# Performance work log

Measured on AMD Instinct MI355X. Metric: run time of the kernel, lower is better.

## Reference

```python
import jax, jax.numpy as jnp
import numpy as np

D_MODEL, HQ, HKV = 2048, 32, 8
DK = D_MODEL // HQ          # 64
GROUP = HQ // HKV           # 4 query heads per kv head
B, S = 1, 2048


def setup_inputs() -> dict:
    key = jax.random.key(0)
    ks = jax.random.split(key, 5)
    sc = 0.02
    return {
        "x":  jax.random.normal(ks[0], (B, S, D_MODEL), jnp.float32),
        "wq": jax.random.normal(ks[1], (D_MODEL, D_MODEL), jnp.float32) * sc,
        "bq": jnp.zeros((D_MODEL,), jnp.float32),
        "wk": jax.random.normal(ks[2], (HKV * DK, D_MODEL), jnp.float32) * sc,
        "bk": jnp.zeros((HKV * DK,), jnp.float32),
        "wv": jax.random.normal(ks[3], (HKV * DK, D_MODEL), jnp.float32) * sc,
        "bv": jnp.zeros((HKV * DK,), jnp.float32),
        "wo": jax.random.normal(ks[4], (D_MODEL, D_MODEL), jnp.float32) * sc,
        "bo": jnp.zeros((D_MODEL,), jnp.float32),
    }


def reference(x, wq, bq, wk, bk, wv, bv, wo, bo):
    b, s, _ = x.shape
    scale = 1.0 / jnp.sqrt(jnp.asarray(DK, x.dtype))
    # projections (torch Linear: y = x @ W.T + b)
    q = (x @ wq.T + bq).reshape(b, s, HKV, GROUP, DK)   # [B,S,Hkv,G,Dk]
    k = (x @ wk.T + bk).reshape(b, s, HKV, DK)          # [B,S,Hkv,Dk]
    v = (x @ wv.T + bv).reshape(b, s, HKV, DK)
    # GQA: broadcast each kv head over its GROUP query heads (no repeat_interleave)
    scores = jnp.einsum("bshgd,bthd->bhgst", q, k) * scale   # [B,Hkv,G,S,S]
    causal = jnp.tril(jnp.ones((s, s), bool))
    scores = jnp.where(causal, scores, jnp.asarray(-jnp.inf, scores.dtype))
    attn = jax.nn.softmax(scores, axis=-1)
    out = jnp.einsum("bhgst,bthd->bshgd", attn, v)           # [B,S,Hkv,G,Dk]
    out = out.reshape(b, s, D_MODEL)
    return out @ wo.T + bo
```

## Files before the change

kernel.cpp:

```cpp
#include <hip/hip_runtime.h>


#define S_LEN 2048
#define DM    2048
#define QKVW  3072

typedef float  f32x4  __attribute__((ext_vector_type(4)));
typedef float  f32x16 __attribute__((ext_vector_type(16)));
typedef __bf16 bf16x8 __attribute__((ext_vector_type(8)));
typedef unsigned short u16;
typedef unsigned int   u32;
typedef u16 u16x8 __attribute__((ext_vector_type(8)));
typedef u32 u32x4 __attribute__((ext_vector_type(4)));

__device__ __forceinline__ u16 f2b(float f) {
    __bf16 h = (__bf16)f;
    return __builtin_bit_cast(unsigned short, h);
}
__device__ __forceinline__ u32 pk2(float lo, float hi) {
    return (u32)f2b(lo) | ((u32)f2b(hi) << 16);
}
__device__ __forceinline__ float max3f(float a, float b, float c) {
    return fmaxf(fmaxf(a, b), c);
}

#define MFMA16(a, b, c) __builtin_amdgcn_mfma_f32_16x16x32_bf16((a), (b), (c), 0, 0, 0)
#define MFMA32(a, b, c) __builtin_amdgcn_mfma_f32_32x32x16_bf16((a), (b), (c), 0, 0, 0)

__device__ __forceinline__ void gld16(const void* g, void* l) {
    __builtin_amdgcn_global_load_lds(
        (const __attribute__((address_space(1))) void*)g,
        (__attribute__((address_space(3))) void*)l, 16, 0, 0);
}

__global__ __launch_bounds__(256) void cvt5(
    const float* __restrict__ x,  const float* __restrict__ wq,
    const float* __restrict__ wk, const float* __restrict__ wv,
    const float* __restrict__ wo,
    const float* __restrict__ bq, const float* __restrict__ bk,
    const float* __restrict__ bv,
    u16* __restrict__ xb, u16* __restrict__ wqkvb, u16* __restrict__ wob,
    float* __restrict__ bqkv)
{
    if (blockIdx.x == 7168) {
        for (int i = threadIdx.x; i < 3072; i += 256)
            bqkv[i] = (i < 2048) ? bq[i] : (i < 2560 ? bk[i - 2048] : bv[i - 2560]);
        return;
    }
    int i = blockIdx.x * 256 + threadIdx.x;
    const float* s; u16* d; int off;
    if      (i < 524288)  { s = x;  d = xb;    off = i; }
    else if (i < 1048576) { s = wq; d = wqkvb; off = i - 524288; }
    else if (i < 1179648) { s = wk; d = wqkvb + (size_t)2048 * 2048; off = i - 1048576; }
    else if (i < 1310720) { s = wv; d = wqkvb + (size_t)2560 * 2048; off = i - 1179648; }
    else                  { s = wo; d = wob;   off = i - 1310720; }
    const float4* s4 = (const float4*)s;
    float4 a = s4[2 * (size_t)off], b = s4[2 * (size_t)off + 1];
    u16x8 o;
    o[0] = f2b(a.x); o[1] = f2b(a.y); o[2] = f2b(a.z); o[3] = f2b(a.w);
    o[4] = f2b(b.x); o[5] = f2b(b.y); o[6] = f2b(b.z); o[7] = f2b(b.w);
    ((u16x8*)d)[(size_t)off] = o;
}

template <bool OUT_BF16, bool QSCALE>
__global__ __launch_bounds__(256) void gemm_nt64(
    const u16* __restrict__ A, const u16* __restrict__ B,
    const float* __restrict__ bias, void* __restrict__ Cv,
    int N, int K, int nxb)
{
    __shared__ u16 As[2][128 * 32];
    __shared__ u16 Bs[2][64 * 32];
    const int nwg = gridDim.x;
    const int bid = blockIdx.x;
    const int wg  = (bid & 7) * (nwg >> 3) + (bid >> 3);
    const int bm  = (wg / nxb) * 128;
    const int bn  = (wg % nxb) * 64;

    const int tid  = threadIdx.x;
    const int lane = tid & 63;
    const int w    = tid >> 6;
    const int wr   = w >> 1, wc = w & 1;
    const int la = lane & 15, lg = lane >> 4;

    f32x4 acc[4][2] = {};

    char* const abase = (char*)&As[0][0] + w * 1024;
    char* const bbase = (char*)&Bs[0][0] + w * 1024;

    for (int k0 = 0; k0 < K; k0 += 64) {
        #pragma unroll
        for (int i = 0; i < 4; ++i) {
            const int c   = tid + 256 * i;
            const int kh  = c >> 9;
            const int rem = c & 511;
            const int row = rem >> 2;
            const int seg = rem & 3;
            gld16(A + (size_t)(bm + row) * K + k0 + kh * 32 + seg * 8,
                  abase + i * 4096);
        }
        #pragma unroll
        for (int i = 0; i < 2; ++i) {
            const int c   = tid + 256 * i;
            const int kh  = c >> 8;
            const int rem = c & 255;
            const int row = rem >> 2;
            const int seg = rem & 3;
            gld16(B + (size_t)(bn + row) * K + k0 + kh * 32 + seg * 8,
                  bbase + i * 4096);
        }
        __syncthreads();
        #pragma unroll
        for (int kh = 0; kh < 2; ++kh) {
            bf16x8 af[4], bf[2];
            #pragma unroll
            for (int m = 0; m < 4; ++m)
                af[m] = *(const bf16x8*)(&As[kh][0] + (wr * 64 + m * 16 + la) * 32 + lg * 8);
            #pragma unroll
            for (int n = 0; n < 2; ++n)
                bf[n] = *(const bf16x8*)(&Bs[kh][0] + (wc * 32 + n * 16 + la) * 32 + lg * 8);
            #pragma unroll
            for (int m = 0; m < 4; ++m)
                #pragma unroll
                for (int n = 0; n < 2; ++n)
                    acc[m][n] = MFMA16(af[m], bf[n], acc[m][n]);
        }
        __syncthreads();
    }

    #pragma unroll
    for (int m = 0; m < 4; ++m) {
        #pragma unroll
        for (int n = 0; n < 2; ++n) {
            const int col = bn + wc * 32 + n * 16 + la;
            const float bb = bias[col];
            const float osc = (QSCALE && col < 2048) ? 0.180336881f : 1.0f;
            #pragma unroll
            for (int j = 0; j < 4; ++j) {
                const int row = bm + wr * 64 + m * 16 + lg * 4 + j;
                const float v = (acc[m][n][j] + bb) * osc;
                if (OUT_BF16) ((u16*)Cv)[(size_t)row * N + col] = f2b(v);
                else          ((float*)Cv)[(size_t)row * N + col] = v;
            }
        }
    }
}

__global__ __launch_bounds__(256) void kvrepack(const u16* __restrict__ QKVb,
                                                u16* __restrict__ Kp,
                                                u16* __restrict__ Vt) {
    const int h   = blockIdx.y;
    const int kt  = blockIdx.x;
    const int tid = threadIdx.x;
    __shared__ u16 T[64][72];
    #pragma unroll
    for (int p = 0; p < 2; ++p) {
        const int idx = p * 256 + tid;
        const int r   = idx >> 3;
        const int c8  = (idx & 7) * 8;
        *(u16x8*)&Kp[((size_t)h * S_LEN + kt * 64 + r) * 64 + c8] =
            *(const u16x8*)&QKVb[(size_t)(kt * 64 + r) * QKVW + 2048 + h * 64 + c8];
    }
    #pragma unroll
    for (int p = 0; p < 2; ++p) {
        const int r  = p * 32 + (tid >> 3);
        const int cs = (tid & 7) * 8;
        u16x8 v = *(const u16x8*)&QKVb[(size_t)(kt * 64 + r) * QKVW + 2560 + h * 64 + cs];
        #pragma unroll
        for (int j = 0; j < 8; ++j) T[r][cs + j] = v[j];
    }
    __syncthreads();
    #pragma unroll
    for (int p = 0; p < 2; ++p) {
        const int d  = p * 32 + (tid >> 3);
        const int ks = (tid & 7) * 8;
        u16x8 o;
        #pragma unroll
        for (int j = 0; j < 8; ++j) o[j] = T[ks + j][d];
        *(u16x8*)&Vt[((size_t)h * 64 + d) * S_LEN + kt * 64 + ks] = o;
    }
}

__global__ __launch_bounds__(512, 4) void attn(
    const u16* __restrict__ Qb,
    const u16* __restrict__ Kp,
    const u16* __restrict__ Vt,
    u16* __restrict__ Ob)
{
    const int tid  = threadIdx.x;
    const int lane = tid & 63;
    const int w    = tid >> 6;
    const int head = w & 3;
    const int par  = w >> 2;
    const int bid  = blockIdx.x;
    const int band = (bid < 256) ? (63 - (bid >> 3)) : ((bid - 256) >> 3);
    const int h    = bid & 7;
    const int hq   = h * 4 + head;
    const int q0   = band * 32;
    const int lq   = lane & 31;
    const int hi   = lane >> 5;

    __shared__ char LDS[65536];

    bf16x8 qf[4];
    #pragma unroll
    for (int ds = 0; ds < 4; ++ds)
        qf[ds] = *(const bf16x8*)&Qb[(size_t)(q0 + lq) * QKVW + hq * 64 + ds * 16 + hi * 8];

    f32x16 ot[2] = {};
    float m = -3e38f, lsum = 0.f;

    const char* Khb = (const char*)(Kp + (size_t)h * S_LEN * 64);
    const char* Vhb = (const char*)(Vt + (size_t)h * 64 * S_LEN);

    const int r0 = tid >> 3;
    const int s0 = (((tid & 7) ^ (r0 & 7)) << 4);
    const int woff = w * 1024;

    const int nch = (band >> 1) + 1;
    const int nit = (nch + 1) >> 1;

    auto stage_pair = [&](int j) {
        const int pb = (j & 1) * 16384;
        const size_t kr = (size_t)(j * 128 + r0);
        gld16(Khb + (kr << 7) + s0,          LDS + pb + woff);
        gld16(Khb + ((kr + 64) << 7) + s0,   LDS + pb + 8192 + woff);
        const size_t vb = ((size_t)r0 << 12) + (size_t)(j * 256) + s0;
        gld16(Vhb + vb,        LDS + 32768 + pb + woff);
        gld16(Vhb + vb + 128,  LDS + 32768 + pb + 8192 + woff);
    };

    stage_pair(0);
    __syncthreads();

    for (int i = 0; i < nit; ++i) {
        if (i + 1 < nit) stage_pair(i + 1);

        const int cg = 2 * i + par;
        if (cg < nch) {
            const int base = (i & 1) * 16384 + par * 8192;
            const char* Kb = LDS + base;
            const char* Vb = LDS + 32768 + base;
            const int k0 = cg * 64;

            f32x16 s[2];
            __builtin_amdgcn_s_setprio(1);
            #pragma unroll
            for (int kt = 0; kt < 2; ++kt) {
                f32x16 acc = {};
                #pragma unroll
                for (int ds = 0; ds < 4; ++ds) {
                    const int key = kt * 32 + lq;
                    const int byteK = (key << 7) + ((ds * 32 + hi * 16) ^ ((key & 7) << 4));
                    bf16x8 kf = *(const bf16x8*)(Kb + byteK);
                    acc = MFMA32(kf, qf[ds], acc);
                }
                s[kt] = acc;
            }
            __builtin_amdgcn_s_setprio(0);

            if (k0 + 63 > q0) {
                #pragma unroll
                for (int kt = 0; kt < 2; ++kt)
                    #pragma unroll
                    for (int r = 0; r < 16; ++r) {
                        const int key = k0 + kt * 32 + (r & 3) + 8 * (r >> 2) + 4 * hi;
                        if (key > q0 + lq) s[kt][r] = -1e30f;
                    }
            }

            float t10[11];
            #pragma unroll
            for (int r = 0; r < 10; ++r)
                t10[r] = max3f(s[(3*r) >> 4][(3*r) & 15],
                               s[(3*r+1) >> 4][(3*r+1) & 15],
                               s[(3*r+2) >> 4][(3*r+2) & 15]);
            t10[10] = fmaxf(s[1][14], s[1][15]);
            const float x0 = max3f(t10[0], t10[1], t10[2]);
            const float x1 = max3f(t10[3], t10[4], t10[5]);
            const float x2 = max3f(t10[6], t10[7], t10[8]);
            const float x3 = fmaxf(t10[9], t10[10]);
            float pm = fmaxf(max3f(x0, x1, x2), x3);
            pm = fmaxf(pm, __shfl_xor(pm, 32));

            if (!__all(pm <= m + 11.5f)) {
                const float mn   = fmaxf(m, pm);
                const float corr = __builtin_exp2f(m - mn);
                m = mn;
                lsum *= corr;
                #pragma unroll
                for (int r = 0; r < 16; ++r) {
                    const int row = (r & 3) + 8 * (r >> 2) + 4 * hi;
                    const float cr = __shfl(corr, row);
                    ot[0][r] *= cr;
                    ot[1][r] *= cr;
                }
            }

            float ps = 0.f;
            #pragma unroll
            for (int kt = 0; kt < 2; ++kt)
                #pragma unroll
                for (int r = 0; r < 16; ++r) {
                    const float p = __builtin_exp2f(s[kt][r] - m);
                    s[kt][r] = p;
                    ps += p;
                }
            lsum += ps + __shfl_xor(ps, 32);

            bf16x8 pa[4];
            #pragma unroll
            for (int kb = 0; kb < 4; ++kb) {
                const int kt = kb >> 1;
                const int rb = (kb & 1) * 8;
                const u32 A = pk2(s[kt][rb + 0], s[kt][rb + 1]);
                const u32 B = pk2(s[kt][rb + 4], s[kt][rb + 5]);
                const u32 C = pk2(s[kt][rb + 2], s[kt][rb + 3]);
                const u32 D = pk2(s[kt][rb + 6], s[kt][rb + 7]);
                const u32 sA = __shfl_xor(A, 32), sB = __shfl_xor(B, 32);
                const u32 sC = __shfl_xor(C, 32), sD = __shfl_xor(D, 32);
                u32x4 t4;
                t4[0] = hi ? sB : A;
                t4[1] = hi ? sD : C;
                t4[2] = hi ? B : sA;
                t4[3] = hi ? D : sC;
                pa[kb] = __builtin_bit_cast(bf16x8, t4);
            }

            __builtin_amdgcn_s_setprio(1);
            #pragma unroll
            for (int dt = 0; dt < 2; ++dt)
                #pragma unroll
                for (int kb = 0; kb < 4; ++kb) {
                    const int d = dt * 32 + lq;
                    const int byteV = (d << 7) + ((kb * 32 + hi * 16) ^ ((d & 7) << 4));
                    bf16x8 vf = *(const bf16x8*)(Vb + byteV);
                    ot[dt] = MFMA32(pa[kb], vf, ot[dt]);
                }
            __builtin_amdgcn_s_setprio(0);
        }

        __syncthreads();
    }

    float* Uls = (float*)LDS;
    float* Mls = (float*)(LDS + 32768);
    float* Lls = (float*)(LDS + 33280);

    if (par == 1) {
        #pragma unroll
        for (int r = 0; r < 16; ++r) {
            const int row = (r & 3) + 8 * (r >> 2) + 4 * hi;
            Uls[(head * 32 + row) * 64 + lq]      = ot[0][r];
            Uls[(head * 32 + row) * 64 + 32 + lq] = ot[1][r];
        }
        if (lane < 32) { Mls[head * 32 + lane] = m; Lls[head * 32 + lane] = lsum; }
    }
    __syncthreads();
    if (par == 1) return;

    const float m1  = Mls[head * 32 + lq];
    const float l1  = Lls[head * 32 + lq];
    const float M   = fmaxf(m, m1);
    const float a0  = __builtin_exp2f(m - M);
    const float a1  = __builtin_exp2f(m1 - M);
    const float inv = 1.f / (a0 * lsum + a1 * l1);

    #pragma unroll
    for (int r = 0; r < 16; ++r) {
        const int row = (r & 3) + 8 * (r >> 2) + 4 * hi;
        const float a0r = __shfl(a0, row);
        const float a1r = __shfl(a1, row);
        const float ivr = __shfl(inv, row);
        #pragma unroll
        for (int dt = 0; dt < 2; ++dt) {
            const float u1 = Uls[(head * 32 + row) * 64 + dt * 32 + lq];
            Ob[(size_t)(q0 + row) * DM + hq * 64 + dt * 32 + lq] =
                f2b((a0r * ot[dt][r] + a1r * u1) * ivr);
        }
    }
}

extern "C" void kernel_launch(void* const* d_in, const int* in_sizes, int n_in,
                              void* d_out, int out_size, void* d_ws, size_t ws_size,
                              hipStream_t stream)
{
    const float* x  = (const float*)d_in[0];
    const float* wq = (const float*)d_in[1];
    const float* bq = (const float*)d_in[2];
    const float* wk = (const float*)d_in[3];
    const float* bk = (const float*)d_in[4];
    const float* wv = (const float*)d_in[5];
    const float* bv = (const float*)d_in[6];
    const float* wo = (const float*)d_in[7];
    const float* bo = (const float*)d_in[8];
    float* out = (float*)d_out;

    char* ws = (char*)d_ws;
    u16* xb     = (u16*)(ws);
    u16* wqkvb  = (u16*)(ws + (8u  << 20));
    u16* wob    = (u16*)(ws + (20u << 20));
    u16* QKVb   = (u16*)(ws + (28u << 20));
    float* bqkv = (float*)(ws + (40u << 20));
    u16* Ob = xb;
    u16* Kp = wqkvb;
    u16* Vt = wqkvb + (size_t)2 * 1024 * 1024 / 2;

    cvt5<<<7169, 256, 0, stream>>>(x, wq, wk, wv, wo, bq, bk, bv,
                                   xb, wqkvb, wob, bqkv);
    gemm_nt64<true, true><<<768, 256, 0, stream>>>(
        xb, wqkvb, bqkv, QKVb, QKVW, 2048, QKVW / 64);
    kvrepack<<<dim3(32, 8), 256, 0, stream>>>(QKVb, Kp, Vt);
    attn<<<512, 512, 0, stream>>>(QKVb, Kp, Vt, Ob);
    gemm_nt64<false, false><<<512, 256, 0, stream>>>(
        Ob, wob, bo, out, DM, 2048, DM / 64);
}
```

Before: 137.6 us.

## Read K directly from QKV buffer and use permlane32 swap for half-wave exchanges

Removes the K repack from the repack kernel, so attention stages K tiles straight from the strided QKV projection output (row stride 6144 bytes) instead of a packed per-head copy. Separately, it replaces the cross-half-wave __shfl_xor(…,32) exchanges in the softmax max, sum and P-fragment build with the permlane32_swap builtin when available. This saves a copy pass and some LDS-routed shuffles, but the K loads become strided global reads with less locality.

```diff
diff --git a/kernel.cpp b/kernel.cpp
--- a/kernel.cpp
+++ b/kernel.cpp
@@ -12,6 +12,7 @@
 typedef unsigned int   u32;
 typedef u16 u16x8 __attribute__((ext_vector_type(8)));
 typedef u32 u32x4 __attribute__((ext_vector_type(4)));
+typedef u32 u32x2 __attribute__((ext_vector_type(2)));
 
 __device__ __forceinline__ u16 f2b(float f) {
     __bf16 h = (__bf16)f;
@@ -22,6 +23,28 @@
 }
 __device__ __forceinline__ float max3f(float a, float b, float c) {
     return fmaxf(fmaxf(a, b), c);
+}
+
+__device__ __forceinline__ void xswap(u32 a, u32 b, u32& lo, u32& hi) {
+#if __has_builtin(__builtin_amdgcn_permlane32_swap)
+    u32x2 r = __builtin_amdgcn_permlane32_swap(a, b, false, false);
+    lo = r[0]; hi = r[1];
+#else
+    const int hf = (threadIdx.x & 63) >> 5;
+    const u32 sA = __shfl_xor(a, 32), sB = __shfl_xor(b, 32);
+    lo = hf ? sB : a;
+    hi = hf ? b : sA;
+#endif
+}
+__device__ __forceinline__ float xhalf_max(float x) {
+    u32 xb = __builtin_bit_cast(u32, x), lo, hi;
+    xswap(xb, xb, lo, hi);
+    return fmaxf(__builtin_bit_cast(float, lo), __builtin_bit_cast(float, hi));
+}
+__device__ __forceinline__ float xhalf_sum(float x) {
+    u32 xb = __builtin_bit_cast(u32, x), lo, hi;
+    xswap(xb, xb, lo, hi);
+    return __builtin_bit_cast(float, lo) + __builtin_bit_cast(float, hi);
 }
 
 #define MFMA16(a, b, c) __builtin_amdgcn_mfma_f32_16x16x32_bf16((a), (b), (c), 0, 0, 0)
@@ -145,23 +168,14 @@
     }
 }
 
-__global__ __launch_bounds__(256) void kvrepack(const u16* __restrict__ QKVb,
-                                                u16* __restrict__ Kp,
-                                                u16* __restrict__ Vt) {
+__global__ __launch_bounds__(256) void vrepack(const u16* __restrict__ QKVb,
+                                               u16* __restrict__ Vt) {
     const int h   = blockIdx.y;
     const int kt  = blockIdx.x;
     const int tid = threadIdx.x;
     __shared__ u16 T[64][72];
     #pragma unroll
     for (int p = 0; p < 2; ++p) {
-        const int idx = p * 256 + tid;
-        const int r   = idx >> 3;
-        const int c8  = (idx & 7) * 8;
-        *(u16x8*)&Kp[((size_t)h * S_LEN + kt * 64 + r) * 64 + c8] =
-            *(const u16x8*)&QKVb[(size_t)(kt * 64 + r) * QKVW + 2048 + h * 64 + c8];
-    }
-    #pragma unroll
-    for (int p = 0; p < 2; ++p) {
         const int r  = p * 32 + (tid >> 3);
         const int cs = (tid & 7) * 8;
         u16x8 v = *(const u16x8*)&QKVb[(size_t)(kt * 64 + r) * QKVW + 2560 + h * 64 + cs];
@@ -181,8 +195,7 @@
 }
 
 __global__ __launch_bounds__(512, 4) void attn(
-    const u16* __restrict__ Qb,
-    const u16* __restrict__ Kp,
+    const u16* __restrict__ QKVb,
     const u16* __restrict__ Vt,
     u16* __restrict__ Ob)
 {
@@ -204,12 +217,12 @@
     bf16x8 qf[4];
     #pragma unroll
     for (int ds = 0; ds < 4; ++ds)
-        qf[ds] = *(const bf16x8*)&Qb[(size_t)(q0 + lq) * QKVW + hq * 64 + ds * 16 + hi * 8];
+        qf[ds] = *(const bf16x8*)&QKVb[(size_t)(q0 + lq) * QKVW + hq * 64 + ds * 16 + hi * 8];
 
     f32x16 ot[2] = {};
     float m = -3e38f, lsum = 0.f;
 
-    const char* Khb = (const char*)(Kp + (size_t)h * S_LEN * 64);
+    const char* Khb = (const char*)QKVb + 4096 + h * 128;
     const char* Vhb = (const char*)(Vt + (size_t)h * 64 * S_LEN);
 
     const int r0 = tid >> 3;
@@ -222,8 +235,8 @@
     auto stage_pair = [&](int j) {
         const int pb = (j & 1) * 16384;
         const size_t kr = (size_t)(j * 128 + r0);
-        gld16(Khb + (kr << 7) + s0,          LDS + pb + woff);
-        gld16(Khb + ((kr + 64) << 7) + s0,   LDS + pb + 8192 + woff);
+        gld16(Khb + kr * 6144 + s0,          LDS + pb + woff);
+        gld16(Khb + (kr + 64) * 6144 + s0,   LDS + pb + 8192 + woff);
         const size_t vb = ((size_t)r0 << 12) + (size_t)(j * 256) + s0;
         gld16(Vhb + vb,        LDS + 32768 + pb + woff);
         gld16(Vhb + vb + 128,  LDS + 32768 + pb + 8192 + woff);
@@ -279,8 +292,7 @@
             const float x1 = max3f(t10[3], t10[4], t10[5]);
             const float x2 = max3f(t10[6], t10[7], t10[8]);
             const float x3 = fmaxf(t10[9], t10[10]);
-            float pm = fmaxf(max3f(x0, x1, x2), x3);
-            pm = fmaxf(pm, __shfl_xor(pm, 32));
+            const float pm = xhalf_max(fmaxf(max3f(x0, x1, x2), x3));
 
             if (!__all(pm <= m + 11.5f)) {
                 const float mn   = fmaxf(m, pm);
@@ -305,7 +317,7 @@
                     s[kt][r] = p;
                     ps += p;
                 }
-            lsum += ps + __shfl_xor(ps, 32);
+            lsum += xhalf_sum(ps);
 
             bf16x8 pa[4];
             #pragma unroll
@@ -316,13 +328,11 @@
                 const u32 B = pk2(s[kt][rb + 4], s[kt][rb + 5]);
                 const u32 C = pk2(s[kt][rb + 2], s[kt][rb + 3]);
                 const u32 D = pk2(s[kt][rb + 6], s[kt][rb + 7]);
-                const u32 sA = __shfl_xor(A, 32), sB = __shfl_xor(B, 32);
-                const u32 sC = __shfl_xor(C, 32), sD = __shfl_xor(D, 32);
+                u32 e0, e1, e2, e3;
+                xswap(A, B, e0, e2);
+                xswap(C, D, e1, e3);
                 u32x4 t4;
-                t4[0] = hi ? sB : A;
-                t4[1] = hi ? sD : C;
-                t4[2] = hi ? B : sA;
-                t4[3] = hi ? D : sC;
+                t4[0] = e0; t4[1] = e1; t4[2] = e2; t4[3] = e3;
                 pa[kb] = __builtin_bit_cast(bf16x8, t4);
             }
 
@@ -402,15 +412,14 @@
     u16* QKVb   = (u16*)(ws + (28u << 20));
     float* bqkv = (float*)(ws + (40u << 20));
     u16* Ob = xb;
-    u16* Kp = wqkvb;
-    u16* Vt = wqkvb + (size_t)2 * 1024 * 1024 / 2;
+    u16* Vt = wqkvb;
 
     cvt5<<<7169, 256, 0, stream>>>(x, wq, wk, wv, wo, bq, bk, bv,
                                    xb, wqkvb, wob, bqkv);
     gemm_nt64<true, true><<<768, 256, 0, stream>>>(
         xb, wqkvb, bqkv, QKVb, QKVW, 2048, QKVW / 64);
-    kvrepack<<<dim3(32, 8), 256, 0, stream>>>(QKVb, Kp, Vt);
-    attn<<<512, 512, 0, stream>>>(QKVb, Kp, Vt, Ob);
+    vrepack<<<dim3(32, 8), 256, 0, stream>>>(QKVb, Vt);
+    attn<<<512, 512, 0, stream>>>(QKVb, Vt, Ob);
     gemm_nt64<false, false><<<512, 256, 0, stream>>>(
         Ob, wob, bo, out, DM, 2048, DM / 64);
 }
```

After: 131.8 us. -4.2%, faster.
